# Kernel tuning notes

Measured on AMD Instinct MI355X. Metric: run time of the kernel, lower is better.

The kernel has to match this reference:

```python
import jax, jax.numpy as jnp
import numpy as np

N_NODES = 50000
N_EDGES = 800000
N_S = 32          # 0e channels in node feats
N_V = 16          # 1o channels in node feats
NB = 8            # radial bessel basis size
H = 64            # MLP hidden
S_OUT = N_S + N_V           # 48 scalar message channels (filtered 0e + dot path)
V_OUT = N_V + N_S + N_V     # 64 vector message channels (filtered 1o + sxY1 + vxY2)
NUM_IRREPS = S_OUT + V_OUT  # 112, gated by radial MLP
AVG_NEIGH = 16.0


def setup_inputs() -> dict:
    key = jax.random.key(0)
    ks = jax.random.split(key, 8)
    # scale so edge lengths fall mostly inside the envelope cutoff x_max=1
    vectors = jax.random.normal(ks[0], (N_EDGES, 3), jnp.float32) * 0.25
    node_s = jax.random.normal(ks[1], (N_NODES, N_S), jnp.float32)
    node_v = jax.random.normal(ks[2], (N_NODES, N_V, 3), jnp.float32)
    senders = jax.random.randint(ks[3], (N_EDGES,), 0, N_NODES)
    receivers = jax.random.randint(ks[4], (N_EDGES,), 0, N_NODES)
    W0 = jax.random.normal(ks[5], (NB, H), jnp.float32)
    W1 = jax.random.normal(ks[6], (H, H), jnp.float32)
    W2 = jax.random.normal(ks[7], (H, NUM_IRREPS), jnp.float32)
    return {"vectors": vectors, "node_s": node_s, "node_v": node_v,
            "W0": W0, "W1": W1, "W2": W2,
            "senders": senders, "receivers": receivers}


def _radial_embed(r):
    # r: [E,1] edge lengths. Bessel basis (x_max=1) * polynomial envelope, 0 at r==0.
    n = jnp.arange(1, NB + 1, dtype=r.dtype)            # [NB]
    safe_r = jnp.maximum(r, 1e-12)
    basis = jnp.sqrt(2.0) * jnp.sin(jnp.pi * n * r) / safe_r   # [E,NB]
    x = r
    env = (1.0 - 28.0 * x**6 + 48.0 * x**7 - 21.0 * x**8) * (x < 1.0)  # smooth cutoff
    return jnp.where(r == 0.0, 0.0, basis * env)        # [E,NB]


def reference(vectors, node_s, node_v, W0, W1, W2, senders, receivers):
    E = vectors.shape[0]
    r = jnp.linalg.norm(vectors, axis=-1, keepdims=True)          # [E,1]
    u = vectors / jnp.maximum(r, 1e-12)                            # unit vectors [E,3]

    # gather sender features
    s = node_s[senders]                                            # [E,N_S]
    v = node_v[senders]                                            # [E,N_V,3]

    # equivariant tensor-product paths against spherical harmonics of u
    # (filtered to target irreps 0e,1o). Y1 ~ u, Y2 ~ traceless u u^T.
    path_a = s[:, :, None] * u[:, None, :]                         # 0e x Y1 -> 1o [E,N_S,3]
    path_b = jnp.einsum('eci,ei->ec', v, u)                        # 1o x Y1 -> 0e [E,N_V]
    T = u[:, :, None] * u[:, None, :] - jnp.eye(3, dtype=u.dtype) / 3.0  # [E,3,3]
    path_c = jnp.sqrt(1.5) * jnp.einsum('eij,ecj->eci', T, v)      # 1o x Y2 -> 1o [E,N_V,3]

    msg_s = jnp.concatenate([s, path_b], axis=-1)                  # [E,S_OUT]
    msg_v = jnp.concatenate([v, path_a, path_c], axis=1)           # [E,V_OUT,3]

    # radial MLP gate (no bias, fan-in scaled, swish hidden, linear output)
    emb = _radial_embed(r)                                         # [E,NB]
    h = jax.nn.swish(emb @ W0 / jnp.sqrt(jnp.asarray(NB, emb.dtype)))
    h = jax.nn.swish(h @ W1 / jnp.sqrt(jnp.asarray(H, emb.dtype)))
    mix = h @ W2 / jnp.sqrt(jnp.asarray(H, emb.dtype))             # [E,NUM_IRREPS]

    msg_s = msg_s * mix[:, :S_OUT]
    msg_v = msg_v * mix[:, S_OUT:, None]

    # scatter-add to receivers
    n = node_s.shape[0]
    out_s = jnp.zeros((n, S_OUT), msg_s.dtype).at[receivers].add(msg_s)
    out_v = jnp.zeros((n, V_OUT, 3), msg_v.dtype).at[receivers].add(msg_v)

    inv = 1.0 / jnp.sqrt(AVG_NEIGH)
    return jnp.concatenate([out_s * inv, (out_v * inv).reshape(n, V_OUT * 3)], axis=-1)
```

## Files before the change

kernel.cpp:

```cpp
#include <hip/hip_runtime.h>
#include <hip/hip_fp16.h>

#define N_S 32
#define N_V 16
#define NB 8
#define HH 64
#define NIR 112
#define ROW 240

typedef __attribute__((ext_vector_type(8))) short short8;
typedef _Float16 half8 __attribute__((ext_vector_type(8)));
typedef float f32x4 __attribute__((ext_vector_type(4)));

__device__ __forceinline__ float swishf(float x) {
  return x / (1.f + __expf(-x));
}

struct ChanDesc { int path, off, mixI, i; };

__device__ __forceinline__ void mkDesc(int t, ChanDesc& d) {
  if (t < 32) { d.path = 0; d.off = t; d.mixI = t; d.i = 0; }
  else if (t < 48) { d.path = 1; d.off = 3 * (t - 32); d.mixI = t; d.i = 0; }
  else if (t < ROW) {
    int q = t - 48, c = q / 3, i = q - 3 * c;
    d.mixI = 48 + c;
    if (c < 16) { d.path = 2; d.off = q; d.i = 0; }
    else if (c < 48) { d.path = 3; d.off = c - 16; d.i = i; }
    else { d.path = 4; d.off = 3 * (c - 48); d.i = i; }
  } else { d.path = -1; d.off = 0; d.mixI = 0; d.i = 0; }
}

__device__ __forceinline__ float evalChan(const ChanDesc& d,
                                          const float* __restrict__ srow,
                                          const float* __restrict__ vrow,
                                          float mix,
                                          float u0, float u1, float u2) {
  if (d.path < 0) return 0.f;
  if (d.path == 0) return srow[d.off] * mix;
  if (d.path == 2) return vrow[d.off] * mix;
  float uo = d.i == 0 ? u0 : (d.i == 1 ? u1 : u2);
  if (d.path == 3) return srow[d.off] * uo * mix;
  float dd = vrow[d.off] * u0 + vrow[d.off + 1] * u1 + vrow[d.off + 2] * u2;
  if (d.path == 1) return dd * mix;
  return 1.22474487139f * (uo * dd - vrow[d.off + d.i] * 0.33333333333f) * mix;
}

__device__ __forceinline__ void radialEmb(float x, float y, float z, bool valid,
                                          float* emb, float* u0, float* u1, float* u2) {
  float r2 = x * x + y * y + z * z;
  float r = sqrtf(r2);
  float invr = 1.f / fmaxf(r, 1e-12f);
  *u0 = x * invr; *u1 = y * invr; *u2 = z * invr;
  float env = 0.f;
  if (r < 1.f) {
    float r3 = r * r2;
    float r6 = r3 * r3;
    env = 1.f + r6 * (-28.f + (48.f - 21.f * r) * r);
  }
  float coef = 1.41421356237f * invr * env;
  if (!valid || r == 0.f) coef = 0.f;
  float ph = 3.14159265358979323846f * r;
  float s1 = __sinf(ph), c1 = __cosf(ph);
  float twc = 2.f * c1;
  float sp = 0.f, sc = s1;
#pragma unroll
  for (int n = 0; n < NB; ++n) {
    emb[n] = coef * sc;
    float sn = twc * sc - sp;
    sp = sc;
    sc = sn;
  }
}


__global__ __launch_bounds__(256) void hist_kernel(const int* __restrict__ rcv,
                                                   int* __restrict__ hist, int E) {
  int e = blockIdx.x * 256 + threadIdx.x;
  if (e < E) atomicAdd(&hist[rcv[e]], 1);
}

__global__ __launch_bounds__(256) void scan1_kernel(const int* __restrict__ hist,
                                                    int* __restrict__ scanTmp,
                                                    int* __restrict__ bsum, int N) {
  __shared__ int sh[256];
  int t = threadIdx.x;
  int i = blockIdx.x * 256 + t;
  sh[t] = (i < N) ? hist[i] : 0;
  __syncthreads();
#pragma unroll
  for (int off = 1; off < 256; off <<= 1) {
    int x = (t >= off) ? sh[t - off] : 0;
    __syncthreads();
    sh[t] += x;
    __syncthreads();
  }
  if (i < N) scanTmp[i] = sh[t];
  if (t == 255) bsum[blockIdx.x] = sh[255];
}

__global__ __launch_bounds__(256) void scan2_kernel(int* __restrict__ bsum, int nb) {
  __shared__ int sh[256];
  int t = threadIdx.x;
  sh[t] = (t < nb) ? bsum[t] : 0;
  __syncthreads();
#pragma unroll
  for (int off = 1; off < 256; off <<= 1) {
    int x = (t >= off) ? sh[t - off] : 0;
    __syncthreads();
    sh[t] += x;
    __syncthreads();
  }
  int excl = (t == 0) ? 0 : sh[t - 1];
  if (t < nb) bsum[t] = excl;
}

__global__ __launch_bounds__(256) void scan3_kernel(const int* __restrict__ scanTmp,
                                                    const int* __restrict__ bsum,
                                                    const int* __restrict__ hist,
                                                    int* __restrict__ offs,
                                                    int* __restrict__ cursor, int N) {
  int i = blockIdx.x * 256 + threadIdx.x;
  if (i < N) {
    int incl = scanTmp[i] + bsum[blockIdx.x];
    offs[i + 1] = incl;
    cursor[i] = incl - hist[i];
    if (i == 0) offs[0] = 0;
  }
}

__global__ __launch_bounds__(256) void reorder_kernel(const int* __restrict__ rcv,
                                                      int* __restrict__ cursor,
                                                      int* __restrict__ sortedE, int E) {
  int e = blockIdx.x * 256 + threadIdx.x;
  if (e < E) {
    int pos = atomicAdd(&cursor[rcv[e]], 1);
    sortedE[pos] = e;
  }
}


__global__ __launch_bounds__(256) void wconv2_kernel(const float* __restrict__ W1,
                                                     const float* __restrict__ W2,
                                                     _Float16* __restrict__ W1T,
                                                     _Float16* __restrict__ W2T) {
  int i = blockIdx.x * 256 + threadIdx.x;
  if (i < 4096) {
    int k = i >> 6, n = i & 63;
    W1T[n * 64 + k] = (_Float16)(W1[k * 64 + n] * 0.125f);
  } else if (i < 4096 + 7168) {
    int j = i - 4096;
    int k = j / 112, n = j - k * 112;
    W2T[n * 64 + k] = (_Float16)(W2[k * 112 + n] * 0.125f);
  }
}

__global__ __launch_bounds__(256, 4) void mlp_mfma_kernel(
    const float* __restrict__ vec,
    const float* __restrict__ W0,
    const _Float16* __restrict__ W1T,
    const _Float16* __restrict__ W2T,
    __half* __restrict__ mixOut,
    int E) {
  __shared__ __align__(16) _Float16 hbuf[4 * 64 * 72];
  const int lane = threadIdx.x & 63;
  const int wave = threadIdx.x >> 6;
  const int gbase = blockIdx.x * 256 + wave * 64;
  _Float16* hb = hbuf + wave * (64 * 72);

  const int m15 = lane & 15;
  const int q = lane >> 4;

  {
    int e = gbase + lane;
    bool valid = e < E;
    float x = 0.f, y = 0.f, z = 0.f;
    if (valid) {
      const float* vp = vec + 3 * (size_t)e;
      x = vp[0]; y = vp[1]; z = vp[2];
    }
    float emb[NB], u0, u1, u2;
    radialEmb(x, y, z, valid, emb, &u0, &u1, &u2);
    for (int kg = 0; kg < 8; ++kg) {
      half8 pk;
#pragma unroll
      for (int kk = 0; kk < 8; ++kk) {
        int k = kg * 8 + kk;
        float a = 0.f;
#pragma unroll
        for (int n = 0; n < NB; ++n) a = fmaf(emb[n], W0[n * HH + k], a);
        pk[kk] = (_Float16)swishf(a * 0.35355339059f);
      }
      *(half8*)(hb + lane * 72 + kg * 8) = pk;
    }
  }

  half8 bW1[4][2];
#pragma unroll
  for (int nt = 0; nt < 4; ++nt)
#pragma unroll
    for (int q2 = 0; q2 < 2; ++q2)
      bW1[nt][q2] = *(const half8*)(W1T + (nt * 16 + m15) * 64 + q2 * 32 + q * 8);

#pragma unroll
  for (int t = 0; t < 4; ++t) {
    half8 a0 = *(const half8*)(hb + (t * 16 + m15) * 72 + q * 8);
    half8 a1 = *(const half8*)(hb + (t * 16 + m15) * 72 + 32 + q * 8);
#pragma unroll
    for (int nt = 0; nt < 4; ++nt) {
      f32x4 d = {0.f, 0.f, 0.f, 0.f};
      d = __builtin_amdgcn_mfma_f32_16x16x32_f16(a0, bW1[nt][0], d, 0, 0, 0);
      d = __builtin_amdgcn_mfma_f32_16x16x32_f16(a1, bW1[nt][1], d, 0, 0, 0);
#pragma unroll
      for (int r = 0; r < 4; ++r)
        hb[(t * 16 + q * 4 + r) * 72 + nt * 16 + m15] = (_Float16)swishf(d[r]);
    }
  }

  half8 A2[4][2];
#pragma unroll
  for (int t = 0; t < 4; ++t)
#pragma unroll
    for (int q2 = 0; q2 < 2; ++q2)
      A2[t][q2] = *(const half8*)(hb + (t * 16 + m15) * 72 + q2 * 32 + q * 8);

  for (int hf = 0; hf < 2; ++hf) {
    const int ntCount = hf ? 3 : 4;
    for (int nl = 0; nl < ntCount; ++nl) {
      int ntg = hf * 4 + nl;
      half8 b0 = *(const half8*)(W2T + (ntg * 16 + m15) * 64 + q * 8);
      half8 b1 = *(const half8*)(W2T + (ntg * 16 + m15) * 64 + 32 + q * 8);
#pragma unroll
      for (int t = 0; t < 4; ++t) {
        f32x4 d = {0.f, 0.f, 0.f, 0.f};
        d = __builtin_amdgcn_mfma_f32_16x16x32_f16(A2[t][0], b0, d, 0, 0, 0);
        d = __builtin_amdgcn_mfma_f32_16x16x32_f16(A2[t][1], b1, d, 0, 0, 0);
#pragma unroll
        for (int r = 0; r < 4; ++r)
          hb[(t * 16 + q * 4 + r) * 72 + nl * 16 + m15] = (_Float16)d[r];
      }
    }
    if (hf == 0) {
      for (int it = 0; it < 8; ++it) {
        int c = it * 64 + lane;
        int el = c >> 3, p = c & 7;
        int e = gbase + el;
        half8 v = *(const half8*)(hb + el * 72 + p * 8);
        if (e < E) *(half8*)((_Float16*)mixOut + (size_t)e * NIR + p * 8) = v;
      }
    } else {
      for (int it = 0; it < 6; ++it) {
        int c = it * 64 + lane;
        int el = (int)(((unsigned)c * 43691u) >> 18);
        int p = c - el * 6;
        int e = gbase + el;
        half8 v = *(const half8*)(hb + el * 72 + p * 8);
        if (e < E) *(half8*)((_Float16*)mixOut + (size_t)e * NIR + 64 + p * 8) = v;
      }
    }
  }
}


__global__ __launch_bounds__(256) void gather_kernel(
    const float* __restrict__ vec,
    const float* __restrict__ nodes_s,
    const float* __restrict__ nodes_v,
    const int* __restrict__ senders,
    const int* __restrict__ offs,
    const int* __restrict__ sortedE,
    const __half* __restrict__ mix,
    float* __restrict__ out, int N) {
  int wid = blockIdx.x * 4 + (threadIdx.x >> 6);
  int lane = threadIdx.x & 63;
  if (wid >= N) return;

  ChanDesc d[4];
#pragma unroll
  for (int tb = 0; tb < 4; ++tb) mkDesc(tb * 64 + lane, d[tb]);

  float acc[4] = {0.f, 0.f, 0.f, 0.f};
  int s0 = offs[wid], s1 = offs[wid + 1];

  for (int i = s0; i < s1; ++i) {
    int e = __builtin_amdgcn_readfirstlane(sortedE[i]);
    int snd = __builtin_amdgcn_readfirstlane(senders[e]);
    const float* vp = vec + 3 * (size_t)e;
    float x = vp[0], y = vp[1], z = vp[2];
    float r = sqrtf(x * x + y * y + z * z);
    float invr = 1.f / fmaxf(r, 1e-12f);
    float u0 = x * invr, u1 = y * invr, u2 = z * invr;
    const float* srow = nodes_s + (size_t)snd * N_S;
    const float* vrow = nodes_v + (size_t)snd * (N_V * 3);
    const __half* mrow = mix + (size_t)e * NIR;
#pragma unroll
    for (int tb = 0; tb < 4; ++tb) {
      if (d[tb].path >= 0) {
        float m = __half2float(mrow[d[tb].mixI]);
        acc[tb] += evalChan(d[tb], srow, vrow, m, u0, u1, u2);
      }
    }
  }

  float* orow = out + (size_t)wid * ROW;
#pragma unroll
  for (int tb = 0; tb < 4; ++tb) {
    int t = tb * 64 + lane;
    if (t < ROW) orow[t] = 0.25f * acc[tb];
  }
}


__global__ __launch_bounds__(64) void edge_kernel(
    const float* __restrict__ vec,
    const float* __restrict__ nodes_s,
    const float* __restrict__ nodes_v,
    const int* __restrict__ senders,
    const int* __restrict__ receivers,
    const float* __restrict__ W0f,
    const float* __restrict__ W1f,
    const float* __restrict__ W2f,
    float* __restrict__ out,
    int E) {
  __shared__ float hLds[HH * 64];
  __shared__ float uLds[64 * 3];
  __shared__ int sLds[64];
  __shared__ int rLds[64];
  __half* mixLds = reinterpret_cast<__half*>(hLds);

  const int lane = threadIdx.x;
  const int base = blockIdx.x * 64;
  const int eg = base + lane;
  const bool valid = eg < E;

  float emb[NB];
  {
    float x = 0.f, y = 0.f, z = 0.f;
    int snd = 0, rcv = 0;
    if (valid) {
      const float* vp = vec + 3 * (size_t)eg;
      x = vp[0]; y = vp[1]; z = vp[2];
      snd = senders[eg];
      rcv = receivers[eg];
    }
    float u0, u1, u2;
    radialEmb(x, y, z, valid, emb, &u0, &u1, &u2);
    uLds[lane * 3 + 0] = u0;
    uLds[lane * 3 + 1] = u1;
    uLds[lane * 3 + 2] = u2;
    sLds[lane] = snd;
    rLds[lane] = rcv;
  }

  for (int j0 = 0; j0 < HH; j0 += 8) {
    float a[8];
#pragma unroll
    for (int jj = 0; jj < 8; ++jj) a[jj] = 0.f;
#pragma unroll
    for (int k = 0; k < NB; ++k) {
      const float* wrow = W0f + k * HH + j0;
      float ek = emb[k];
#pragma unroll
      for (int jj = 0; jj < 8; ++jj) a[jj] = fmaf(ek, wrow[jj], a[jj]);
    }
#pragma unroll
    for (int jj = 0; jj < 8; ++jj)
      hLds[(j0 + jj) * 64 + lane] = swishf(a[jj] * 0.35355339059f);
  }
  __syncthreads();

  float h2[HH];
#pragma unroll
  for (int j = 0; j < HH; ++j) h2[j] = 0.f;
  for (int k = 0; k < HH; ++k) {
    float hk = hLds[k * 64 + lane];
    const float* wrow = W1f + k * HH;
#pragma unroll
    for (int j = 0; j < HH; ++j) h2[j] = fmaf(hk, wrow[j], h2[j]);
  }
#pragma unroll
  for (int j = 0; j < HH; ++j) h2[j] = swishf(h2[j] * 0.125f);
  __syncthreads();

  for (int m0 = 0; m0 < NIR; m0 += 4) {
    float a0 = 0.f, a1 = 0.f, a2 = 0.f, a3 = 0.f;
#pragma unroll
    for (int k = 0; k < HH; ++k) {
      const float* wrow = W2f + k * NIR + m0;
      float hk = h2[k];
      a0 = fmaf(hk, wrow[0], a0);
      a1 = fmaf(hk, wrow[1], a1);
      a2 = fmaf(hk, wrow[2], a2);
      a3 = fmaf(hk, wrow[3], a3);
    }
    mixLds[lane * NIR + m0 + 0] = __float2half_rn(a0 * 0.125f);
    mixLds[lane * NIR + m0 + 1] = __float2half_rn(a1 * 0.125f);
    mixLds[lane * NIR + m0 + 2] = __float2half_rn(a2 * 0.125f);
    mixLds[lane * NIR + m0 + 3] = __float2half_rn(a3 * 0.125f);
  }
  __syncthreads();

  ChanDesc d[4];
#pragma unroll
  for (int tb = 0; tb < 4; ++tb) mkDesc(tb * 64 + lane, d[tb]);

  const int cnt = min(64, E - base);
  for (int e = 0; e < cnt; ++e) {
    int snd = sLds[e], rcv = rLds[e];
    float u0 = uLds[e * 3 + 0], u1 = uLds[e * 3 + 1], u2 = uLds[e * 3 + 2];
    const float* srow = nodes_s + (size_t)snd * N_S;
    const float* vrow = nodes_v + (size_t)snd * (N_V * 3);
    const __half* mrow = mixLds + e * NIR;
    float* orow = out + (size_t)rcv * ROW;
#pragma unroll
    for (int tb = 0; tb < 4; ++tb) {
      if (d[tb].path >= 0) {
        float m = __half2float(mrow[d[tb].mixI]);
        float val = evalChan(d[tb], srow, vrow, m, u0, u1, u2);
        unsafeAtomicAdd(orow + tb * 64 + lane, 0.25f * val);
      }
    }
  }
}


extern "C" void kernel_launch(void* const* d_in, const int* in_sizes, int n_in,
                              void* d_out, int out_size, void* d_ws, size_t ws_size,
                              hipStream_t stream) {
  const float* vec = (const float*)d_in[0];
  const float* ns = (const float*)d_in[1];
  const float* nv = (const float*)d_in[2];
  const float* w0 = (const float*)d_in[3];
  const float* w1 = (const float*)d_in[4];
  const float* w2 = (const float*)d_in[5];
  const int* snd = (const int*)d_in[6];
  const int* rcv = (const int*)d_in[7];
  float* out = (float*)d_out;

  const int E = in_sizes[6];
  const int N = in_sizes[1] / N_S;
  const int nb = (N + 255) / 256;
  const int eb = (E + 255) / 256;

  char* p = (char*)d_ws;
  __half* mixW = (__half*)p;      p += (size_t)E * NIR * sizeof(__half);
  int* hist = (int*)p;            p += (size_t)N * 4;
  int* scanTmp = (int*)p;         p += (size_t)N * 4;
  int* offs = (int*)p;            p += ((size_t)N + 1) * 4;
  int* cursor = (int*)p;          p += (size_t)N * 4;
  int* bsum = (int*)p;            p += 256 * 4;
  int* sortedE = (int*)p;         p += (size_t)E * 4;
  p = (char*)(((uintptr_t)p + 15) & ~(uintptr_t)15);
  _Float16* W1T = (_Float16*)p;   p += 4096 * sizeof(_Float16);
  _Float16* W2T = (_Float16*)p;   p += 7168 * sizeof(_Float16);
  size_t need = (size_t)(p - (char*)d_ws);

  if (need <= ws_size && nb <= 256) {
    hipMemsetAsync(hist, 0, (size_t)N * 4, stream);
    hist_kernel<<<eb, 256, 0, stream>>>(rcv, hist, E);
    scan1_kernel<<<nb, 256, 0, stream>>>(hist, scanTmp, bsum, N);
    scan2_kernel<<<1, 256, 0, stream>>>(bsum, nb);
    scan3_kernel<<<nb, 256, 0, stream>>>(scanTmp, bsum, hist, offs, cursor, N);
    reorder_kernel<<<eb, 256, 0, stream>>>(rcv, cursor, sortedE, E);
    wconv2_kernel<<<44, 256, 0, stream>>>(w1, w2, W1T, W2T);
    mlp_mfma_kernel<<<eb, 256, 0, stream>>>(vec, w0, W1T, W2T, mixW, E);
    gather_kernel<<<(N + 3) / 4, 256, 0, stream>>>(vec, ns, nv, snd, offs, sortedE, mixW, out, N);
  } else {
    hipMemsetAsync(d_out, 0, (size_t)out_size * sizeof(float), stream);
    edge_kernel<<<(E + 63) / 64, 64, 0, stream>>>(vec, ns, nv, snd, rcv, w0, w1, w2, out, E);
  }
}
```

Before: 630.9 us.

## Scatter MLP outputs into receiver-sorted rows with fp16 node features

The MLP kernel now writes each edge's gate row, unit vector and sender index straight to that edge's receiver-sorted position, using an inverse permutation, into a padded 120-half row. The gather kernel then reads mix rows contiguously instead of indirecting through a sorted edge list and recomputing unit vectors. Node features are converted to fp16 up front so the per-edge sender gathers move half the bytes. This adds a conversion kernel and scattered writes in the MLP stage, and node features lose precision to fp16.

Result: slower. 661.4 us (+4.8%).

```diff
diff --git a/kernel.cpp b/kernel.cpp
--- a/kernel.cpp
+++ b/kernel.cpp
@@ -7,8 +7,8 @@
 #define HH 64
 #define NIR 112
 #define ROW 240
-
-typedef __attribute__((ext_vector_type(8))) short short8;
+#define MROW 120
+
 typedef _Float16 half8 __attribute__((ext_vector_type(8)));
 typedef float f32x4 __attribute__((ext_vector_type(4)));
 
@@ -33,8 +33,7 @@
 __device__ __forceinline__ float evalChan(const ChanDesc& d,
                                           const float* __restrict__ srow,
                                           const float* __restrict__ vrow,
-                                          float mix,
-                                          float u0, float u1, float u2) {
+                                          float mix, float u0, float u1, float u2) {
   if (d.path < 0) return 0.f;
   if (d.path == 0) return srow[d.off] * mix;
   if (d.path == 2) return vrow[d.off] * mix;
@@ -43,6 +42,19 @@
   float dd = vrow[d.off] * u0 + vrow[d.off + 1] * u1 + vrow[d.off + 2] * u2;
   if (d.path == 1) return dd * mix;
   return 1.22474487139f * (uo * dd - vrow[d.off + d.i] * 0.33333333333f) * mix;
+}
+
+__device__ __forceinline__ float evalChan16(const ChanDesc& d,
+                                            const _Float16* __restrict__ srow,
+                                            const _Float16* __restrict__ vrow,
+                                            float mix, float u0, float u1, float u2) {
+  if (d.path == 0) return (float)srow[d.off] * mix;
+  if (d.path == 2) return (float)vrow[d.off] * mix;
+  float uo = d.i == 0 ? u0 : (d.i == 1 ? u1 : u2);
+  if (d.path == 3) return (float)srow[d.off] * uo * mix;
+  float dd = (float)vrow[d.off] * u0 + (float)vrow[d.off + 1] * u1 + (float)vrow[d.off + 2] * u2;
+  if (d.path == 1) return dd * mix;
+  return 1.22474487139f * (uo * dd - (float)vrow[d.off + d.i] * 0.33333333333f) * mix;
 }
 
 __device__ __forceinline__ void radialEmb(float x, float y, float z, bool valid,
@@ -135,6 +147,16 @@
   if (e < E) {
     int pos = atomicAdd(&cursor[rcv[e]], 1);
     sortedE[pos] = e;
+  }
+}
+
+__global__ __launch_bounds__(256) void reorderInv_kernel(const int* __restrict__ rcv,
+                                                         int* __restrict__ cursor,
+                                                         int* __restrict__ invPos, int E) {
+  int e = blockIdx.x * 256 + threadIdx.x;
+  if (e < E) {
+    int pos = atomicAdd(&cursor[rcv[e]], 1);
+    invPos[e] = pos;
   }
 }
 
@@ -154,12 +176,25 @@
   }
 }
 
-__global__ __launch_bounds__(256, 4) void mlp_mfma_kernel(
+__global__ __launch_bounds__(256) void nodeconv_kernel(const float* __restrict__ ns,
+                                                       const float* __restrict__ nv,
+                                                       _Float16* __restrict__ s16,
+                                                       _Float16* __restrict__ v16, int N) {
+  int i = blockIdx.x * 256 + threadIdx.x;
+  int ts = N * N_S;
+  int tv = N * N_V * 3;
+  if (i < ts) s16[i] = (_Float16)ns[i];
+  else if (i < ts + tv) v16[i - ts] = (_Float16)nv[i - ts];
+}
+
+__global__ __launch_bounds__(256, 4) void mlp_mfma_sorted_kernel(
     const float* __restrict__ vec,
     const float* __restrict__ W0,
     const _Float16* __restrict__ W1T,
     const _Float16* __restrict__ W2T,
-    __half* __restrict__ mixOut,
+    const int* __restrict__ senders,
+    const int* __restrict__ invPos,
+    _Float16* __restrict__ mixS,
     int E) {
   __shared__ __align__(16) _Float16 hbuf[4 * 64 * 72];
   const int lane = threadIdx.x & 63;
@@ -167,6 +202,182 @@
   const int gbase = blockIdx.x * 256 + wave * 64;
   _Float16* hb = hbuf + wave * (64 * 72);
 
+  const int m15 = lane & 15;
+  const int q = lane >> 4;
+
+  {
+    int e = gbase + lane;
+    bool valid = e < E;
+    float x = 0.f, y = 0.f, z = 0.f;
+    int snd = 0;
+    if (valid) {
+      const float* vp = vec + 3 * (size_t)e;
+      x = vp[0]; y = vp[1]; z = vp[2];
+      snd = senders[e];
+    }
+    float emb[NB], u0, u1, u2;
+    radialEmb(x, y, z, valid, emb, &u0, &u1, &u2);
+    for (int kg = 0; kg < 8; ++kg) {
+      half8 pk;
+#pragma unroll
+      for (int kk = 0; kk < 8; ++kk) {
+        int k = kg * 8 + kk;
+        float a = 0.f;
+#pragma unroll
+        for (int n = 0; n < NB; ++n) a = fmaf(emb[n], W0[n * HH + k], a);
+        pk[kk] = (_Float16)swishf(a * 0.35355339059f);
+      }
+      *(half8*)(hb + lane * 72 + kg * 8) = pk;
+    }
+    float* auxp = (float*)(hb + lane * 72 + 64);
+    auxp[0] = u0; auxp[1] = u1; auxp[2] = u2;
+    ((int*)auxp)[3] = snd;
+  }
+
+  half8 bW1[4][2];
+#pragma unroll
+  for (int nt = 0; nt < 4; ++nt)
+#pragma unroll
+    for (int q2 = 0; q2 < 2; ++q2)
+      bW1[nt][q2] = *(const half8*)(W1T + (nt * 16 + m15) * 64 + q2 * 32 + q * 8);
+
+#pragma unroll
+  for (int t = 0; t < 4; ++t) {
+    half8 a0 = *(const half8*)(hb + (t * 16 + m15) * 72 + q * 8);
+    half8 a1 = *(const half8*)(hb + (t * 16 + m15) * 72 + 32 + q * 8);
+#pragma unroll
+    for (int nt = 0; nt < 4; ++nt) {
+      f32x4 d = {0.f, 0.f, 0.f, 0.f};
+      d = __builtin_amdgcn_mfma_f32_16x16x32_f16(a0, bW1[nt][0], d, 0, 0, 0);
+      d = __builtin_amdgcn_mfma_f32_16x16x32_f16(a1, bW1[nt][1], d, 0, 0, 0);
+#pragma unroll
+      for (int r = 0; r < 4; ++r)
+        hb[(t * 16 + q * 4 + r) * 72 + nt * 16 + m15] = (_Float16)swishf(d[r]);
+    }
+  }
+
+  half8 A2[4][2];
+#pragma unroll
+  for (int t = 0; t < 4; ++t)
+#pragma unroll
+    for (int q2 = 0; q2 < 2; ++q2)
+      A2[t][q2] = *(const half8*)(hb + (t * 16 + m15) * 72 + q2 * 32 + q * 8);
+
+  for (int nl = 0; nl < 4; ++nl) {
+    half8 b0 = *(const half8*)(W2T + (nl * 16 + m15) * 64 + q * 8);
+    half8 b1 = *(const half8*)(W2T + (nl * 16 + m15) * 64 + 32 + q * 8);
+#pragma unroll
+    for (int t = 0; t < 4; ++t) {
+      f32x4 d = {0.f, 0.f, 0.f, 0.f};
+      d = __builtin_amdgcn_mfma_f32_16x16x32_f16(A2[t][0], b0, d, 0, 0, 0);
+      d = __builtin_amdgcn_mfma_f32_16x16x32_f16(A2[t][1], b1, d, 0, 0, 0);
+#pragma unroll
+      for (int r = 0; r < 4; ++r)
+        hb[(t * 16 + q * 4 + r) * 72 + nl * 16 + m15] = (_Float16)d[r];
+    }
+  }
+  for (int it = 0; it < 8; ++it) {
+    int c = it * 64 + lane;
+    int el = c >> 3, p = c & 7;
+    int e = gbase + el;
+    half8 v = *(const half8*)(hb + el * 72 + p * 8);
+    if (e < E) {
+      int pos = invPos[e];
+      *(half8*)(mixS + (size_t)pos * MROW + p * 8) = v;
+    }
+  }
+
+  for (int nl = 0; nl < 3; ++nl) {
+    int ntg = 4 + nl;
+    half8 b0 = *(const half8*)(W2T + (ntg * 16 + m15) * 64 + q * 8);
+    half8 b1 = *(const half8*)(W2T + (ntg * 16 + m15) * 64 + 32 + q * 8);
+#pragma unroll
+    for (int t = 0; t < 4; ++t) {
+      f32x4 d = {0.f, 0.f, 0.f, 0.f};
+      d = __builtin_amdgcn_mfma_f32_16x16x32_f16(A2[t][0], b0, d, 0, 0, 0);
+      d = __builtin_amdgcn_mfma_f32_16x16x32_f16(A2[t][1], b1, d, 0, 0, 0);
+#pragma unroll
+      for (int r = 0; r < 4; ++r)
+        hb[(t * 16 + q * 4 + r) * 72 + nl * 16 + m15] = (_Float16)d[r];
+    }
+  }
+  for (int it = 0; it < 7; ++it) {
+    int c = it * 64 + lane;
+    int el = (int)(((unsigned)c * 9363u) >> 16);
+    int p = c - el * 7;
+    int e = gbase + el;
+    half8 v = *(const half8*)(hb + el * 72 + (p < 6 ? p * 8 : 64));
+    if (e < E) {
+      int pos = invPos[e];
+      *(half8*)(mixS + (size_t)pos * MROW + 64 + p * 8) = v;
+    }
+  }
+}
+
+
+__device__ __forceinline__ void gstep(int i, const _Float16* __restrict__ mixS,
+                                      const _Float16* __restrict__ s16,
+                                      const _Float16* __restrict__ v16,
+                                      const ChanDesc* __restrict__ d, float* __restrict__ acc) {
+  const _Float16* row = mixS + (size_t)i * MROW;
+  float4 aux = *(const float4*)(const void*)(row + 112);
+  int snd = __float_as_int(aux.w);
+  const _Float16* srow = s16 + (size_t)snd * N_S;
+  const _Float16* vrow = v16 + (size_t)snd * (N_V * 3);
+#pragma unroll
+  for (int tb = 0; tb < 4; ++tb) {
+    if (d[tb].path >= 0) {
+      float m = (float)row[d[tb].mixI];
+      acc[tb] += evalChan16(d[tb], srow, vrow, m, aux.x, aux.y, aux.z);
+    }
+  }
+}
+
+__global__ __launch_bounds__(256) void gather_sorted_kernel(
+    const _Float16* __restrict__ mixS,
+    const _Float16* __restrict__ s16,
+    const _Float16* __restrict__ v16,
+    const int* __restrict__ offs,
+    float* __restrict__ out, int N) {
+  int wid = blockIdx.x * 4 + (threadIdx.x >> 6);
+  int lane = threadIdx.x & 63;
+  if (wid >= N) return;
+
+  ChanDesc d[4];
+#pragma unroll
+  for (int tb = 0; tb < 4; ++tb) mkDesc(tb * 64 + lane, d[tb]);
+
+  float acc[4] = {0.f, 0.f, 0.f, 0.f};
+  int s0 = __builtin_amdgcn_readfirstlane(offs[wid]);
+  int s1 = __builtin_amdgcn_readfirstlane(offs[wid + 1]);
+
+  int i = s0;
+  for (; i + 2 <= s1; i += 2) {
+    gstep(i, mixS, s16, v16, d, acc);
+    gstep(i + 1, mixS, s16, v16, d, acc);
+  }
+  if (i < s1) gstep(i, mixS, s16, v16, d, acc);
+
+  float* orow = out + (size_t)wid * ROW;
+#pragma unroll
+  for (int tb = 0; tb < 4; ++tb) {
+    int t = tb * 64 + lane;
+    if (t < ROW) orow[t] = 0.25f * acc[tb];
+  }
+}
+
+
+__global__ __launch_bounds__(256, 4) void mlp_mfma_kernel(
+    const float* __restrict__ vec,
+    const float* __restrict__ W0,
+    const _Float16* __restrict__ W1T,
+    const _Float16* __restrict__ W2T,
+    __half* __restrict__ mixOut, int E) {
+  __shared__ __align__(16) _Float16 hbuf[4 * 64 * 72];
+  const int lane = threadIdx.x & 63;
+  const int wave = threadIdx.x >> 6;
+  const int gbase = blockIdx.x * 256 + wave * 64;
+  _Float16* hb = hbuf + wave * (64 * 72);
   const int m15 = lane & 15;
   const int q = lane >> 4;
 
@@ -260,7 +471,6 @@
   }
 }
 
-
 __global__ __launch_bounds__(256) void gather_kernel(
     const float* __restrict__ vec,
     const float* __restrict__ nodes_s,
@@ -319,8 +529,7 @@
     const float* __restrict__ W0f,
     const float* __restrict__ W1f,
     const float* __restrict__ W2f,
-    float* __restrict__ out,
-    int E) {
+    float* __restrict__ out, int E) {
   __shared__ float hLds[HH * 64];
   __shared__ float uLds[64 * 3];
   __shared__ int sLds[64];
@@ -441,31 +650,65 @@
   const int nb = (N + 255) / 256;
   const int eb = (E + 255) / 256;
 
-  char* p = (char*)d_ws;
-  __half* mixW = (__half*)p;      p += (size_t)E * NIR * sizeof(__half);
-  int* hist = (int*)p;            p += (size_t)N * 4;
-  int* scanTmp = (int*)p;         p += (size_t)N * 4;
-  int* offs = (int*)p;            p += ((size_t)N + 1) * 4;
-  int* cursor = (int*)p;          p += (size_t)N * 4;
-  int* bsum = (int*)p;            p += 256 * 4;
-  int* sortedE = (int*)p;         p += (size_t)E * 4;
-  p = (char*)(((uintptr_t)p + 15) & ~(uintptr_t)15);
-  _Float16* W1T = (_Float16*)p;   p += 4096 * sizeof(_Float16);
-  _Float16* W2T = (_Float16*)p;   p += 7168 * sizeof(_Float16);
-  size_t need = (size_t)(p - (char*)d_ws);
-
-  if (need <= ws_size && nb <= 256) {
-    hipMemsetAsync(hist, 0, (size_t)N * 4, stream);
-    hist_kernel<<<eb, 256, 0, stream>>>(rcv, hist, E);
-    scan1_kernel<<<nb, 256, 0, stream>>>(hist, scanTmp, bsum, N);
-    scan2_kernel<<<1, 256, 0, stream>>>(bsum, nb);
-    scan3_kernel<<<nb, 256, 0, stream>>>(scanTmp, bsum, hist, offs, cursor, N);
-    reorder_kernel<<<eb, 256, 0, stream>>>(rcv, cursor, sortedE, E);
-    wconv2_kernel<<<44, 256, 0, stream>>>(w1, w2, W1T, W2T);
-    mlp_mfma_kernel<<<eb, 256, 0, stream>>>(vec, w0, W1T, W2T, mixW, E);
-    gather_kernel<<<(N + 3) / 4, 256, 0, stream>>>(vec, ns, nv, snd, offs, sortedE, mixW, out, N);
-  } else {
-    hipMemsetAsync(d_out, 0, (size_t)out_size * sizeof(float), stream);
-    edge_kernel<<<(E + 63) / 64, 64, 0, stream>>>(vec, ns, nv, snd, rcv, w0, w1, w2, out, E);
-  }
-}
+  {
+    char* p = (char*)d_ws;
+    _Float16* mixS = (_Float16*)p; p += (size_t)E * MROW * sizeof(_Float16);
+    int* hist = (int*)p;           p += (size_t)N * 4;
+    int* scanTmp = (int*)p;        p += (size_t)N * 4;
+    int* offs = (int*)p;           p += ((size_t)N + 1) * 4;
+    int* cursor = (int*)p;         p += (size_t)N * 4;
+    int* bsum = (int*)p;           p += 256 * 4;
+    int* invPos = (int*)p;         p += (size_t)E * 4;
+    p = (char*)(((uintptr_t)p + 15) & ~(uintptr_t)15);
+    _Float16* W1T = (_Float16*)p;  p += 4096 * sizeof(_Float16);
+    _Float16* W2T = (_Float16*)p;  p += 7168 * sizeof(_Float16);
+    _Float16* s16 = (_Float16*)p;  p += (size_t)N * N_S * sizeof(_Float16);
+    _Float16* v16 = (_Float16*)p;  p += (size_t)N * N_V * 3 * sizeof(_Float16);
+    size_t needA = (size_t)(p - (char*)d_ws);
+
+    if (needA <= ws_size && nb <= 256) {
+      hipMemsetAsync(hist, 0, (size_t)N * 4, stream);
+      hist_kernel<<<eb, 256, 0, stream>>>(rcv, hist, E);
+      scan1_kernel<<<nb, 256, 0, stream>>>(hist, scanTmp, bsum, N);
+      scan2_kernel<<<1, 256, 0, stream>>>(bsum, nb);
+      scan3_kernel<<<nb, 256, 0, stream>>>(scanTmp, bsum, hist, offs, cursor, N);
+      reorderInv_kernel<<<eb, 256, 0, stream>>>(rcv, cursor, invPos, E);
+      wconv2_kernel<<<44, 256, 0, stream>>>(w1, w2, W1T, W2T);
+      nodeconv_kernel<<<(N * 80 + 255) / 256, 256, 0, stream>>>(ns, nv, s16, v16, N);
+      mlp_mfma_sorted_kernel<<<eb, 256, 0, stream>>>(vec, w0, W1T, W2T, snd, invPos, mixS, E);
+      gather_sorted_kernel<<<(N + 3) / 4, 256, 0, stream>>>(mixS, s16, v16, offs, out, N);
+      return;
+    }
+  }
+
+  {
+    char* p = (char*)d_ws;
+    __half* mixW = (__half*)p;     p += (size_t)E * NIR * sizeof(__half);
+    int* hist = (int*)p;           p += (size_t)N * 4;
+    int* scanTmp = (int*)p;        p += (size_t)N * 4;
+    int* offs = (int*)p;           p += ((size_t)N + 1) * 4;
+    int* cursor = (int*)p;         p += (size_t)N * 4;
+    int* bsum = (int*)p;           p += 256 * 4;
+    int* sortedE = (int*)p;        p += (size_t)E * 4;
+    p = (char*)(((uintptr_t)p + 15) & ~(uintptr_t)15);
+    _Float16* W1T = (_Float16*)p;  p += 4096 * sizeof(_Float16);
+    _Float16* W2T = (_Float16*)p;  p += 7168 * sizeof(_Float16);
+    size_t needB = (size_t)(p - (char*)d_ws);
+
+    if (needB <= ws_size && nb <= 256) {
+      hipMemsetAsync(hist, 0, (size_t)N * 4, stream);
+      hist_kernel<<<eb, 256, 0, stream>>>(rcv, hist, E);
+      scan1_kernel<<<nb, 256, 0, stream>>>(hist, scanTmp, bsum, N);
+      scan2_kernel<<<1, 256, 0, stream>>>(bsum, nb);
+      scan3_kernel<<<nb, 256, 0, stream>>>(scanTmp, bsum, hist, offs, cursor, N);
+      reorder_kernel<<<eb, 256, 0, stream>>>(rcv, cursor, sortedE, E);
+      wconv2_kernel<<<44, 256, 0, stream>>>(w1, w2, W1T, W2T);
+      mlp_mfma_kernel<<<eb, 256, 0, stream>>>(vec, w0, W1T, W2T, mixW, E);
+      gather_kernel<<<(N + 3) / 4, 256, 0, stream>>>(vec, ns, nv, snd, offs, sortedE, mixW, out, N);
+      return;
+    }
+  }
+
+  hipMemsetAsync(d_out, 0, (size_t)out_size * sizeof(float), stream);
+  edge_kernel<<<(E + 63) / 64, 64, 0, stream>>>(vec, ns, nv, snd, rcv, w0, w1, w2, out, E);
+}
```
